# Optimization experiments

Hardware: AMD Instinct MI355X
Metric: run time of the kernel (lower is better)

The kernel has to match this reference:

```python
import jax, jax.numpy as jnp
import numpy as np

B, T, L, INPUT_DIM = 16, 128, 100, 100
EMB = 100
FEAT = INPUT_DIM + 3 * EMB          # 400
HID, OUT = 128, 50
RNN_IN = 2 * INPUT_DIM + 3 * L      # 500
VOCAB = 10000 + 2


def setup_inputs() -> dict:
    key = jax.random.key(0)
    ks = jax.random.split(key, 12)
    first = jax.random.normal(ks[0], (B, T, INPUT_DIM), jnp.float32)
    idx = jax.random.randint(ks[1], (B, T, 3 * L), 0, VOCAB).astype(jnp.float32)
    x = jnp.concatenate([first, idx], axis=2)  # [B,T,400]
    s = 0.05
    return {
        "x": x,
        "embed_nodes": jax.random.normal(ks[2], (VOCAB, EMB), jnp.float32) * s,
        "embed_paths": jax.random.normal(ks[3], (VOCAB, EMB), jnp.float32) * s,
        "W_t": jax.random.normal(ks[4], (FEAT, FEAT), jnp.float32) / np.sqrt(FEAT),
        "b_t": jnp.zeros((FEAT,), jnp.float32),
        "W_a": jax.random.normal(ks[5], (FEAT, 1), jnp.float32) / np.sqrt(FEAT),
        "b_a": jnp.zeros((1,), jnp.float32),
        "W_ih": jax.random.normal(ks[6], (4 * HID, RNN_IN), jnp.float32) / np.sqrt(RNN_IN),
        "W_hh": jax.random.normal(ks[7], (4 * HID, HID), jnp.float32) / np.sqrt(HID),
        "b_ih": jnp.zeros((4 * HID,), jnp.float32),
        "b_hh": jnp.zeros((4 * HID,), jnp.float32),
        "W_fc": jax.random.normal(ks[8], (HID, OUT), jnp.float32) / np.sqrt(HID),
        "b_fc": jnp.zeros((OUT,), jnp.float32),
    }


def _lstm(xs, W_ih, W_hh, b_ih, b_hh):
    # xs: [B,T,D] -> out [B,T,H]; PyTorch gate order i,f,g,o
    def step(carry, xt):
        h, c = carry
        g = xt @ W_ih.T + h @ W_hh.T + (b_ih + b_hh)  # [B,4H]
        i, f, gg, o = jnp.split(g, 4, axis=-1)
        c = jax.nn.sigmoid(f) * c + jax.nn.sigmoid(i) * jnp.tanh(gg)
        h = jax.nn.sigmoid(o) * jnp.tanh(c)
        return (h, c), h
    h0 = jnp.zeros((xs.shape[0], HID), xs.dtype)
    (_, _), hs = jax.lax.scan(step, (h0, h0), jnp.swapaxes(xs, 0, 1))
    return jnp.swapaxes(hs, 0, 1)


def reference(x, embed_nodes, embed_paths, W_t, b_t, W_a, b_a,
              W_ih, W_hh, b_ih, b_hh, W_fc, b_fc):
    first = x[:, :, :INPUT_DIM]                                   # [B,T,100]
    c2v = x[:, :, INPUT_DIM:INPUT_DIM + 3 * L].reshape(B, T, L, 3).astype(jnp.int32)
    s_emb = embed_nodes[c2v[..., 0]]                              # [B,T,L,100]
    e_emb = embed_nodes[c2v[..., 2]]
    p_emb = embed_paths[c2v[..., 1]]
    att_part = jnp.broadcast_to(first[:, :, None, :], (B, T, L, INPUT_DIM))
    full = jnp.concatenate([s_emb, e_emb, p_emb, att_part], axis=3)  # [B,T,L,400]
    # dropout skipped (deterministic reference == evaluating=True path)
    transformed = jnp.tanh(full @ W_t + b_t)
    ctx = transformed @ W_a + b_a                                 # [B,T,L,1]
    # faithful to nn.Softmax(dim=1): softmax over the sequence axis T
    attn = jax.nn.softmax(ctx, axis=1)
    code_vectors = jnp.sum(full * attn, axis=2)                   # [B,T,400]
    rnn_input = jnp.concatenate([first, code_vectors], axis=2)    # [B,T,500]
    out = _lstm(rnn_input, W_ih, W_hh, b_ih, b_hh)                # [B,T,128]
    return jax.nn.sigmoid(out @ W_fc + b_fc)                      # [B,T,50]
```

## Files before the change

kernel.cpp:

```cpp
#include <hip/hip_runtime.h>
#include <hip/hip_bf16.h>
#include <stdint.h>

#define B_     16
#define T_     128
#define L_     100
#define IN_    100
#define EMB_   100
#define FEAT_  400
#define HID_   128
#define OUT_   50
#define RNNIN_ 500
#define VOCAB_ 10002
#define BT_    2048
#define TBLK   157

#define S_T    (0.16f / 127.0f)
#define INVS_T (127.0f / 0.16f)

typedef __attribute__((ext_vector_type(8))) short short8;
typedef __attribute__((ext_vector_type(4))) float f32x4;

__device__ __forceinline__ float fast_tanh(float x) {
    x = fminf(15.f, fmaxf(-15.f, x));
    float e = __expf(2.f * x);
    return (e - 1.f) * __builtin_amdgcn_rcpf(e + 1.f);
}
__device__ __forceinline__ float sigm(float x) {
    x = fminf(30.f, fmaxf(-30.f, x));
    float e = __expf(-x);
    return __builtin_amdgcn_rcpf(1.f + e);
}
__device__ __forceinline__ signed char q8(float v, float invs) {
    float t = fminf(127.f, fmaxf(-127.f, v * invs));
    return (signed char)__float2int_rn(t);
}
__device__ __forceinline__ int sb(unsigned int u, int k) {
    return (int)(signed char)(u >> (8 * k));
}

__global__ __launch_bounds__(256) void casts_k(
    const float* __restrict__ Wt, const float* __restrict__ Wih,
    const float* __restrict__ Whh,
    __hip_bfloat16* __restrict__ WtT, __hip_bfloat16* __restrict__ Wih_bf,
    __hip_bfloat16* __restrict__ Whh_bf)
{
    int t0 = blockIdx.x * 256 + threadIdx.x;
    const int stride = 256 * 256;
    for (int i = t0; i < 4 * 400 * 128; i += stride) {
        int w = i / (400 * 128), rem = i - w * 400 * 128;
        int n = rem >> 7, k = rem & 127;
        WtT[i] = __float2bfloat16((k < 100) ? Wt[(size_t)(w * 100 + k) * 400 + n] : 0.f);
    }
    for (int i = t0; i < 512 * 512; i += stride) {
        int g = i >> 9, k = i & 511;
        Wih_bf[i] = __float2bfloat16((k < 500) ? Wih[(size_t)g * 500 + k] : 0.f);
    }
    for (int i = t0; i < 512 * 128; i += stride) Whh_bf[i] = __float2bfloat16(Whh[i]);
}

__device__ __forceinline__ void load_a100_f32(const float* __restrict__ arow,
                                              int kg, short8 af[4])
{
#pragma unroll
    for (int s = 0; s < 3; s++) {
        const float* p = arow + s * 32 + kg * 8;
#pragma unroll
        for (int j = 0; j < 8; j++)
            af[s][j] = (short)__bfloat16_as_ushort(__float2bfloat16(p[j]));
    }
    short8 z = {};
    af[3] = z;
    if (kg == 0) {
#pragma unroll
        for (int j = 0; j < 4; j++)
            af[3][j] = (short)__bfloat16_as_ushort(__float2bfloat16(arow[96 + j]));
    }
}

__global__ __launch_bounds__(256) void mm_k(
    const float* __restrict__ EN, const float* __restrict__ EP,
    const float* __restrict__ x, const __hip_bfloat16* __restrict__ WtT,
    const float* __restrict__ btb,
    signed char* __restrict__ Es, signed char* __restrict__ Ee,
    signed char* __restrict__ Ep, float* __restrict__ q)
{
    int blk = blockIdx.x, tid = threadIdx.x;
    int wave = tid >> 6, lane = tid & 63;
    int cl = lane & 15, kg = lane >> 4;

    if (blk < 3 * TBLK) {
        int which = blk / TBLK, mb = blk - which * TBLK;
        const float* A = (which == 2) ? EP : EN;
        signed char* outp = (which == 0) ? Es : ((which == 1) ? Ee : Ep);
        int r0 = mb * 64 + wave * 16;
        int ra = r0 + cl; if (ra > VOCAB_ - 1) ra = VOCAB_ - 1;
        short8 af[4];
        load_a100_f32(A + (size_t)ra * 100, kg, af);
        const __hip_bfloat16* Bp = WtT + (size_t)which * 400 * 128;
        for (int n0 = 0; n0 < 25; n0++) {
            const __hip_bfloat16* brow = Bp + (size_t)(n0 * 16 + cl) * 128 + kg * 8;
            f32x4 acc = (f32x4){0.f, 0.f, 0.f, 0.f};
            acc = __builtin_amdgcn_mfma_f32_16x16x32_bf16(af[0], *(const short8*)(brow), acc, 0, 0, 0);
            acc = __builtin_amdgcn_mfma_f32_16x16x32_bf16(af[1], *(const short8*)(brow + 32), acc, 0, 0, 0);
            acc = __builtin_amdgcn_mfma_f32_16x16x32_bf16(af[2], *(const short8*)(brow + 64), acc, 0, 0, 0);
            acc = __builtin_amdgcn_mfma_f32_16x16x32_bf16(af[3], *(const short8*)(brow + 96), acc, 0, 0, 0);
            int colj = n0 * 16 + cl;
#pragma unroll
            for (int r = 0; r < 4; r++) {
                int gr = r0 + kg * 4 + r;
                if (gr < VOCAB_)
                    outp[(size_t)gr * 400 + colj] = q8(acc[r], INVS_T);
            }
        }
    } else {
        int mb = blk - 3 * TBLK;
        int r0 = mb * 64 + wave * 16;
        short8 af[4];
        load_a100_f32(x + (size_t)(r0 + cl) * 400, kg, af);
        const __hip_bfloat16* Bp = WtT + (size_t)3 * 400 * 128;
        for (int n0 = 0; n0 < 25; n0++) {
            const __hip_bfloat16* brow = Bp + (size_t)(n0 * 16 + cl) * 128 + kg * 8;
            f32x4 acc = (f32x4){0.f, 0.f, 0.f, 0.f};
            acc = __builtin_amdgcn_mfma_f32_16x16x32_bf16(af[0], *(const short8*)(brow), acc, 0, 0, 0);
            acc = __builtin_amdgcn_mfma_f32_16x16x32_bf16(af[1], *(const short8*)(brow + 32), acc, 0, 0, 0);
            acc = __builtin_amdgcn_mfma_f32_16x16x32_bf16(af[2], *(const short8*)(brow + 64), acc, 0, 0, 0);
            acc = __builtin_amdgcn_mfma_f32_16x16x32_bf16(af[3], *(const short8*)(brow + 96), acc, 0, 0, 0);
            int colj = n0 * 16 + cl;
            float bb = btb[colj];
#pragma unroll
            for (int r = 0; r < 4; r++) {
                int gr = r0 + kg * 4 + r;
                q[(size_t)gr * 400 + colj] = acc[r] + bb;
            }
        }
    }
}

__global__ __launch_bounds__(256) void stage_a(
    const float* __restrict__ x,
    const signed char* __restrict__ Es8, const signed char* __restrict__ Ee8,
    const signed char* __restrict__ Ep8,
    const float* __restrict__ q, const float* __restrict__ Wa,
    float* __restrict__ ctx)
{
    __shared__ int idx_s[300];
    int bt = blockIdx.x, tid = threadIdx.x;
    const float* xr = x + (size_t)bt * 400 + 100;
    for (int i = tid; i < 300; i += 256) idx_s[i] = (int)xr[i];
    int lane = tid & 63, wave = tid >> 6;
    bool act = lane < 50;
    int j0 = lane * 8;
    float qv[8], wv[8];
    if (act) {
        float4 qa = *(const float4*)(q + (size_t)bt * 400 + j0);
        float4 qb = *(const float4*)(q + (size_t)bt * 400 + j0 + 4);
        float4 wa = *(const float4*)(Wa + j0);
        float4 wb = *(const float4*)(Wa + j0 + 4);
        qv[0]=qa.x; qv[1]=qa.y; qv[2]=qa.z; qv[3]=qa.w;
        qv[4]=qb.x; qv[5]=qb.y; qv[6]=qb.z; qv[7]=qb.w;
        wv[0]=wa.x; wv[1]=wa.y; wv[2]=wa.z; wv[3]=wa.w;
        wv[4]=wb.x; wv[5]=wb.y; wv[6]=wb.z; wv[7]=wb.w;
    } else {
#pragma unroll
        for (int jj = 0; jj < 8; jj++) { qv[jj] = 0.f; wv[jj] = 0.f; }
    }
    __syncthreads();
    for (int l = wave; l < 100; l += 4) {
        int i0 = idx_s[3 * l], i1 = idx_s[3 * l + 1], i2 = idx_s[3 * l + 2];
        float sum = 0.f;
        if (act) {
            uint2 a  = ((const uint2*)(Es8 + (size_t)i0 * 400))[lane];
            uint2 b  = ((const uint2*)(Ee8 + (size_t)i2 * 400))[lane];
            uint2 cc = ((const uint2*)(Ep8 + (size_t)i1 * 400))[lane];
            int zi[8];
#pragma unroll
            for (int k = 0; k < 4; k++) {
                zi[k]     = sb(a.x, k) + sb(b.x, k) + sb(cc.x, k);
                zi[4 + k] = sb(a.y, k) + sb(b.y, k) + sb(cc.y, k);
            }
#pragma unroll
            for (int jj = 0; jj < 8; jj++) {
                float z = fmaf((float)zi[jj], S_T, qv[jj]);
                sum = fmaf(fast_tanh(z), wv[jj], sum);
            }
        }
#pragma unroll
        for (int off = 32; off; off >>= 1) sum += __shfl_xor(sum, off);
        if (lane == 0) ctx[(size_t)bt * 100 + l] = sum;
    }
}

__global__ __launch_bounds__(256) void softmax_w(
    const float* __restrict__ ctx, float* __restrict__ attn)
{
    int wid = blockIdx.x * 4 + (threadIdx.x >> 6);
    int lane = threadIdx.x & 63;
    int b = wid / 100, l = wid - b * 100;
    size_t base = (size_t)b * 128 * 100 + l;
    float v0 = ctx[base + (size_t)lane * 100];
    float v1 = ctx[base + (size_t)(lane + 64) * 100];
    float m = fmaxf(v0, v1);
#pragma unroll
    for (int off = 32; off; off >>= 1) m = fmaxf(m, __shfl_xor(m, off));
    float e0 = __expf(v0 - m), e1 = __expf(v1 - m);
    float s = e0 + e1;
#pragma unroll
    for (int off = 32; off; off >>= 1) s += __shfl_xor(s, off);
    float rs = 1.f / s;
    attn[base + (size_t)lane * 100] = e0 * rs;
    attn[base + (size_t)(lane + 64) * 100] = e1 * rs;
}

__global__ __launch_bounds__(128) void stage_c(
    const float* __restrict__ x, const float* __restrict__ attn,
    const float* __restrict__ EN, const float* __restrict__ EP,
    __hip_bfloat16* __restrict__ rnn_bf)
{
    __shared__ float at[100];
    __shared__ int idx[300];
    int bt = blockIdx.x, tid = threadIdx.x;
    if (tid < 100) at[tid] = attn[(size_t)bt * 100 + tid];
    const float* xr = x + (size_t)bt * 400 + 100;
    for (int i = tid; i < 300; i += 128) idx[i] = (int)xr[i];
    __syncthreads();
    int d = tid;
    __hip_bfloat16* o = rnn_bf + (size_t)bt * 512;
    if (d < 100) {
        float as = 0.f, ae = 0.f, ap = 0.f, sa = 0.f;
#pragma unroll 4
        for (int l = 0; l < 100; l++) {
            float a = at[l]; sa += a;
            as = fmaf(a, EN[(size_t)idx[3 * l] * 100 + d], as);
            ae = fmaf(a, EN[(size_t)idx[3 * l + 2] * 100 + d], ae);
            ap = fmaf(a, EP[(size_t)idx[3 * l + 1] * 100 + d], ap);
        }
        float fi = x[(size_t)bt * 400 + d];
        o[d]       = __float2bfloat16(fi);
        o[100 + d] = __float2bfloat16(as);
        o[200 + d] = __float2bfloat16(ae);
        o[300 + d] = __float2bfloat16(ap);
        o[400 + d] = __float2bfloat16(fi * sa);
    } else if (d < 112) {
        o[400 + d] = __float2bfloat16(0.f);
    }
}

__global__ __launch_bounds__(256) void gemm_x(
    const __hip_bfloat16* __restrict__ rnn_bf, const __hip_bfloat16* __restrict__ Wih_bf,
    const float* __restrict__ bih, const float* __restrict__ bhh,
    float* __restrict__ X)
{
    int blk = blockIdx.x, tid = threadIdx.x;
    int wave = tid >> 6, lane = tid & 63;
    int cl = lane & 15, kg = lane >> 4;
    int r0 = blk * 64 + wave * 16;

    short8 af[16];
    const __hip_bfloat16* arow = rnn_bf + (size_t)(r0 + cl) * 512 + kg * 8;
#pragma unroll
    for (int ks = 0; ks < 16; ks++) af[ks] = *(const short8*)(arow + ks * 32);

    for (int n0 = 0; n0 < 32; n0 += 2) {
        const __hip_bfloat16* b0 = Wih_bf + (size_t)(n0 * 16 + cl) * 512 + kg * 8;
        const __hip_bfloat16* b1 = b0 + 16 * 512;
        f32x4 acA = (f32x4){0.f, 0.f, 0.f, 0.f};
        f32x4 acB = (f32x4){0.f, 0.f, 0.f, 0.f};
#pragma unroll
        for (int ks = 0; ks < 16; ks++) {
            acA = __builtin_amdgcn_mfma_f32_16x16x32_bf16(af[ks], *(const short8*)(b0 + ks * 32), acA, 0, 0, 0);
            acB = __builtin_amdgcn_mfma_f32_16x16x32_bf16(af[ks], *(const short8*)(b1 + ks * 32), acB, 0, 0, 0);
        }
        int c0 = n0 * 16 + cl, c1 = c0 + 16;
        float bi0 = bih[c0] + bhh[c0];
        float bi1 = bih[c1] + bhh[c1];
#pragma unroll
        for (int r = 0; r < 4; r++) {
            int m = r0 + kg * 4 + r;
            X[(size_t)m * 512 + c0] = acA[r] + bi0;
            X[(size_t)m * 512 + c1] = acB[r] + bi1;
        }
    }
}

__global__ __launch_bounds__(512, 1) void lstm_k(
    const float* __restrict__ X, const __hip_bfloat16* __restrict__ Whh_bf,
    float* __restrict__ hs)
{
    int b = blockIdx.x, tid = threadIdx.x;
    int wave = tid >> 6, lane = tid & 63;
    int col = lane & 15, kg = lane >> 4;

    short8 bf[4][4];
#pragma unroll
    for (int n = 0; n < 4; n++) {
        int g = n * 128 + wave * 16 + col;
#pragma unroll
        for (int kk = 0; kk < 4; kk++)
            bf[n][kk] = *(const short8*)(Whh_bf + (size_t)g * 128 + kk * 32 + kg * 8);
    }

    __shared__ __hip_bfloat16 hbuf[2][128];
    __shared__ float Xs[16][512];
    __shared__ float hsb_s[16][128];
    float c = 0.f;
    if (tid < 128) hbuf[0][tid] = __float2bfloat16(0.f);
    const float* xb = X + (size_t)b * 128 * 512;
    float* hb = hs + (size_t)b * 128 * 128;
    int j = wave * 16 + col;
    int p = 0;

    __syncthreads();

    for (int tc = 0; tc < 8; tc++) {
        {
            const float* src = xb + (size_t)tc * 16 * 512 + tid;
#pragma unroll
            for (int k = 0; k < 16; k++) Xs[k][tid] = src[k * 512];
        }
        __syncthreads();

#pragma unroll 1
        for (int ts = 0; ts < 16; ts++) {
            short8 af[4];
            short8 zz = {};
#pragma unroll
            for (int kk = 0; kk < 4; kk++) {
                af[kk] = zz;
                if (col == 0) af[kk] = *(const short8*)(&hbuf[p][0] + kk * 32 + kg * 8);
            }
            f32x4 acc[4];
#pragma unroll
            for (int n = 0; n < 4; n++) acc[n] = (f32x4){0.f, 0.f, 0.f, 0.f};
#pragma unroll
            for (int kk = 0; kk < 4; kk++)
#pragma unroll
                for (int n = 0; n < 4; n++)
                    acc[n] = __builtin_amdgcn_mfma_f32_16x16x32_bf16(af[kk], bf[n][kk], acc[n], 0, 0, 0);

            if (lane < 16) {
                float pi = acc[0][0] + Xs[ts][j];
                float pf = acc[1][0] + Xs[ts][128 + j];
                float pg = acc[2][0] + Xs[ts][256 + j];
                float po = acc[3][0] + Xs[ts][384 + j];
                c = sigm(pf) * c + sigm(pi) * fast_tanh(pg);
                float hn = sigm(po) * fast_tanh(c);
                hbuf[p ^ 1][j] = __float2bfloat16(hn);
                hsb_s[ts][j] = hn;
            }
            __syncthreads();
            p ^= 1;
        }

        {
            float* dst = hb + (size_t)tc * 16 * 128;
#pragma unroll
            for (int k = 0; k < 4; k++) {
                int i = k * 512 + tid;
                dst[i] = hsb_s[i >> 7][i & 127];
            }
        }
    }
}

__global__ __launch_bounds__(64) void fc_k(
    const float* __restrict__ hs, const float* __restrict__ Wfc,
    const float* __restrict__ bfc, float* __restrict__ out)
{
    int r0 = blockIdx.x * 4, o = threadIdx.x;
    if (o >= 50) return;
    float acc[4] = {0.f, 0.f, 0.f, 0.f};
    for (int j = 0; j < 128; j++) {
        float wv = Wfc[j * 50 + o];
#pragma unroll
        for (int r = 0; r < 4; r++)
            acc[r] = fmaf(hs[(size_t)(r0 + r) * 128 + j], wv, acc[r]);
    }
    float bb = bfc[o];
#pragma unroll
    for (int r = 0; r < 4; r++) out[(size_t)(r0 + r) * 50 + o] = sigm(acc[r] + bb);
}

extern "C" void kernel_launch(void* const* d_in, const int* in_sizes, int n_in,
                              void* d_out, int out_size, void* d_ws, size_t ws_size,
                              hipStream_t stream) {
    const float* x   = (const float*)d_in[0];
    const float* EN  = (const float*)d_in[1];
    const float* EP  = (const float*)d_in[2];
    const float* Wt  = (const float*)d_in[3];
    const float* bt  = (const float*)d_in[4];
    const float* Wa  = (const float*)d_in[5];
    const float* Wih = (const float*)d_in[7];
    const float* Whh = (const float*)d_in[8];
    const float* bih = (const float*)d_in[9];
    const float* bhh = (const float*)d_in[10];
    const float* Wfc = (const float*)d_in[11];
    const float* bfc = (const float*)d_in[12];
    float* out = (float*)d_out;

    char* ws = (char*)d_ws;
    size_t off = 0;
    auto alloc = [&](size_t bytes) -> char* {
        char* p = ws + off;
        off = (off + bytes + 255) & ~(size_t)255;
        return p;
    };
    signed char* Es  = (signed char*)alloc((size_t)VOCAB_ * 400);
    signed char* Ee  = (signed char*)alloc((size_t)VOCAB_ * 400);
    signed char* Epb = (signed char*)alloc((size_t)VOCAB_ * 400);
    __hip_bfloat16* WtT    = (__hip_bfloat16*)alloc((size_t)4 * 400 * 128 * 2);
    __hip_bfloat16* Wih_bf = (__hip_bfloat16*)alloc((size_t)512 * 512 * 2);
    __hip_bfloat16* Whh_bf = (__hip_bfloat16*)alloc((size_t)512 * 128 * 2);
    __hip_bfloat16* rnn_bf = (__hip_bfloat16*)alloc((size_t)BT_ * 512 * 2);
    float* q    = (float*)alloc((size_t)BT_ * 400 * 4);
    float* ctx  = (float*)alloc((size_t)BT_ * 100 * 4);
    float* attn = (float*)alloc((size_t)BT_ * 100 * 4);
    float* X    = (float*)alloc((size_t)BT_ * 512 * 4);
    float* hsb  = (float*)alloc((size_t)BT_ * 128 * 4);

    casts_k<<<256, 256, 0, stream>>>(Wt, Wih, Whh, WtT, Wih_bf, Whh_bf);
    mm_k<<<3 * TBLK + 32, 256, 0, stream>>>(EN, EP, x, WtT, bt,
                                            Es, Ee, Epb, q);
    stage_a<<<BT_, 256, 0, stream>>>(x, Es, Ee, Epb, q, Wa, ctx);
    softmax_w<<<400, 256, 0, stream>>>(ctx, attn);
    stage_c<<<BT_, 128, 0, stream>>>(x, attn, EN, EP, rnn_bf);
    gemm_x<<<32, 256, 0, stream>>>(rnn_bf, Wih_bf, bih, bhh, X);
    lstm_k<<<B_, 512, 0, stream>>>(X, Whh_bf, hsb);
    fc_k<<<BT_ / 4, 64, 0, stream>>>(hsb, Wfc, bfc, out);
}
```

Before: 275.0 us.

## Fold weight casts into mm_k and fuse FC epilogue into LSTM kernel

Removes the separate casts_k launch. mm_k now reads W_t directly as fp32 with strided column loads and converts to bf16 in registers, and extra blocks appended to its grid convert Wih/Whh. The fc_k kernel is removed; each LSTM block stages Wfc in shared memory after the recurrence and computes the sigmoid output for its own batch row. This saves two launches and the WtT round trip, at the cost of uncoalesced strided W_t reads repeated per block and an FC tail running on only 16 blocks.

```diff
diff --git a/kernel.cpp b/kernel.cpp
--- a/kernel.cpp
+++ b/kernel.cpp
@@ -14,6 +14,7 @@
 #define VOCAB_ 10002
 #define BT_    2048
 #define TBLK   157
+#define MMGRID (3 * TBLK + 32 + 64)
 
 #define S_T    (0.16f / 127.0f)
 #define INVS_T (127.0f / 0.16f)
@@ -39,26 +40,6 @@
     return (int)(signed char)(u >> (8 * k));
 }
 
-__global__ __launch_bounds__(256) void casts_k(
-    const float* __restrict__ Wt, const float* __restrict__ Wih,
-    const float* __restrict__ Whh,
-    __hip_bfloat16* __restrict__ WtT, __hip_bfloat16* __restrict__ Wih_bf,
-    __hip_bfloat16* __restrict__ Whh_bf)
-{
-    int t0 = blockIdx.x * 256 + threadIdx.x;
-    const int stride = 256 * 256;
-    for (int i = t0; i < 4 * 400 * 128; i += stride) {
-        int w = i / (400 * 128), rem = i - w * 400 * 128;
-        int n = rem >> 7, k = rem & 127;
-        WtT[i] = __float2bfloat16((k < 100) ? Wt[(size_t)(w * 100 + k) * 400 + n] : 0.f);
-    }
-    for (int i = t0; i < 512 * 512; i += stride) {
-        int g = i >> 9, k = i & 511;
-        Wih_bf[i] = __float2bfloat16((k < 500) ? Wih[(size_t)g * 500 + k] : 0.f);
-    }
-    for (int i = t0; i < 512 * 128; i += stride) Whh_bf[i] = __float2bfloat16(Whh[i]);
-}
-
 __device__ __forceinline__ void load_a100_f32(const float* __restrict__ arow,
                                               int kg, short8 af[4])
 {
@@ -78,12 +59,33 @@
     }
 }
 
+__device__ __forceinline__ void load_b100_f32(const float* __restrict__ colbase,
+                                              int kg, short8 bfr[4])
+{
+#pragma unroll
+    for (int s = 0; s < 3; s++) {
+        const float* p = colbase + (size_t)(s * 32 + kg * 8) * 400;
+#pragma unroll
+        for (int j = 0; j < 8; j++)
+            bfr[s][j] = (short)__bfloat16_as_ushort(__float2bfloat16(p[(size_t)j * 400]));
+    }
+    short8 z = {};
+    bfr[3] = z;
+    if (kg == 0) {
+#pragma unroll
+        for (int j = 0; j < 4; j++)
+            bfr[3][j] = (short)__bfloat16_as_ushort(__float2bfloat16(colbase[(size_t)(96 + j) * 400]));
+    }
+}
+
 __global__ __launch_bounds__(256) void mm_k(
     const float* __restrict__ EN, const float* __restrict__ EP,
-    const float* __restrict__ x, const __hip_bfloat16* __restrict__ WtT,
+    const float* __restrict__ x, const float* __restrict__ Wt,
     const float* __restrict__ btb,
+    const float* __restrict__ Wih, const float* __restrict__ Whh,
     signed char* __restrict__ Es, signed char* __restrict__ Ee,
-    signed char* __restrict__ Ep, float* __restrict__ q)
+    signed char* __restrict__ Ep, float* __restrict__ q,
+    __hip_bfloat16* __restrict__ Wih_bf, __hip_bfloat16* __restrict__ Whh_bf)
 {
     int blk = blockIdx.x, tid = threadIdx.x;
     int wave = tid >> 6, lane = tid & 63;
@@ -97,15 +99,16 @@
         int ra = r0 + cl; if (ra > VOCAB_ - 1) ra = VOCAB_ - 1;
         short8 af[4];
         load_a100_f32(A + (size_t)ra * 100, kg, af);
-        const __hip_bfloat16* Bp = WtT + (size_t)which * 400 * 128;
+        const float* Wslice = Wt + (size_t)(which * 100) * 400;
         for (int n0 = 0; n0 < 25; n0++) {
-            const __hip_bfloat16* brow = Bp + (size_t)(n0 * 16 + cl) * 128 + kg * 8;
+            int colj = n0 * 16 + cl;
+            short8 bfr[4];
+            load_b100_f32(Wslice + colj, kg, bfr);
             f32x4 acc = (f32x4){0.f, 0.f, 0.f, 0.f};
-            acc = __builtin_amdgcn_mfma_f32_16x16x32_bf16(af[0], *(const short8*)(brow), acc, 0, 0, 0);
-            acc = __builtin_amdgcn_mfma_f32_16x16x32_bf16(af[1], *(const short8*)(brow + 32), acc, 0, 0, 0);
-            acc = __builtin_amdgcn_mfma_f32_16x16x32_bf16(af[2], *(const short8*)(brow + 64), acc, 0, 0, 0);
-            acc = __builtin_amdgcn_mfma_f32_16x16x32_bf16(af[3], *(const short8*)(brow + 96), acc, 0, 0, 0);
-            int colj = n0 * 16 + cl;
+            acc = __builtin_amdgcn_mfma_f32_16x16x32_bf16(af[0], bfr[0], acc, 0, 0, 0);
+            acc = __builtin_amdgcn_mfma_f32_16x16x32_bf16(af[1], bfr[1], acc, 0, 0, 0);
+            acc = __builtin_amdgcn_mfma_f32_16x16x32_bf16(af[2], bfr[2], acc, 0, 0, 0);
+            acc = __builtin_amdgcn_mfma_f32_16x16x32_bf16(af[3], bfr[3], acc, 0, 0, 0);
 #pragma unroll
             for (int r = 0; r < 4; r++) {
                 int gr = r0 + kg * 4 + r;
@@ -113,20 +116,21 @@
                     outp[(size_t)gr * 400 + colj] = q8(acc[r], INVS_T);
             }
         }
-    } else {
+    } else if (blk < 3 * TBLK + 32) {
         int mb = blk - 3 * TBLK;
         int r0 = mb * 64 + wave * 16;
         short8 af[4];
         load_a100_f32(x + (size_t)(r0 + cl) * 400, kg, af);
-        const __hip_bfloat16* Bp = WtT + (size_t)3 * 400 * 128;
+        const float* Wslice = Wt + (size_t)300 * 400;
         for (int n0 = 0; n0 < 25; n0++) {
-            const __hip_bfloat16* brow = Bp + (size_t)(n0 * 16 + cl) * 128 + kg * 8;
+            int colj = n0 * 16 + cl;
+            short8 bfr[4];
+            load_b100_f32(Wslice + colj, kg, bfr);
             f32x4 acc = (f32x4){0.f, 0.f, 0.f, 0.f};
-            acc = __builtin_amdgcn_mfma_f32_16x16x32_bf16(af[0], *(const short8*)(brow), acc, 0, 0, 0);
-            acc = __builtin_amdgcn_mfma_f32_16x16x32_bf16(af[1], *(const short8*)(brow + 32), acc, 0, 0, 0);
-            acc = __builtin_amdgcn_mfma_f32_16x16x32_bf16(af[2], *(const short8*)(brow + 64), acc, 0, 0, 0);
-            acc = __builtin_amdgcn_mfma_f32_16x16x32_bf16(af[3], *(const short8*)(brow + 96), acc, 0, 0, 0);
-            int colj = n0 * 16 + cl;
+            acc = __builtin_amdgcn_mfma_f32_16x16x32_bf16(af[0], bfr[0], acc, 0, 0, 0);
+            acc = __builtin_amdgcn_mfma_f32_16x16x32_bf16(af[1], bfr[1], acc, 0, 0, 0);
+            acc = __builtin_amdgcn_mfma_f32_16x16x32_bf16(af[2], bfr[2], acc, 0, 0, 0);
+            acc = __builtin_amdgcn_mfma_f32_16x16x32_bf16(af[3], bfr[3], acc, 0, 0, 0);
             float bb = btb[colj];
 #pragma unroll
             for (int r = 0; r < 4; r++) {
@@ -134,6 +138,16 @@
                 q[(size_t)gr * 400 + colj] = acc[r] + bb;
             }
         }
+    } else {
+        int cb = blk - (3 * TBLK + 32);
+        int t0 = cb * 256 + tid;
+        const int stride = 64 * 256;
+        for (int i = t0; i < 512 * 512; i += stride) {
+            int g = i >> 9, k = i & 511;
+            Wih_bf[i] = __float2bfloat16((k < 500) ? Wih[(size_t)g * 500 + k] : 0.f);
+        }
+        for (int i = t0; i < 512 * 128; i += stride)
+            Whh_bf[i] = __float2bfloat16(Whh[i]);
     }
 }
 
@@ -285,7 +299,8 @@
 
 __global__ __launch_bounds__(512, 1) void lstm_k(
     const float* __restrict__ X, const __hip_bfloat16* __restrict__ Whh_bf,
-    float* __restrict__ hs)
+    const float* __restrict__ Wfc, const float* __restrict__ bfc,
+    float* __restrict__ hs, float* __restrict__ out)
 {
     int b = blockIdx.x, tid = threadIdx.x;
     int wave = tid >> 6, lane = tid & 63;
@@ -361,24 +376,25 @@
             }
         }
     }
-}
-
-__global__ __launch_bounds__(64) void fc_k(
-    const float* __restrict__ hs, const float* __restrict__ Wfc,
-    const float* __restrict__ bfc, float* __restrict__ out)
-{
-    int r0 = blockIdx.x * 4, o = threadIdx.x;
-    if (o >= 50) return;
-    float acc[4] = {0.f, 0.f, 0.f, 0.f};
-    for (int j = 0; j < 128; j++) {
-        float wv = Wfc[j * 50 + o];
-#pragma unroll
-        for (int r = 0; r < 4; r++)
-            acc[r] = fmaf(hs[(size_t)(r0 + r) * 128 + j], wv, acc[r]);
-    }
-    float bb = bfc[o];
-#pragma unroll
-    for (int r = 0; r < 4; r++) out[(size_t)(r0 + r) * 50 + o] = sigm(acc[r] + bb);
+
+    __syncthreads();
+    float* wfc_s = (float*)&Xs[0][0];
+    for (int i = tid; i < 6400; i += 512) wfc_s[i] = Wfc[i];
+    __syncthreads();
+    for (int i = tid; i < 128 * 50; i += 512) {
+        int t = i / 50, o = i - t * 50;
+        float acc = bfc[o];
+        const float4* h4 = (const float4*)(hb + (size_t)t * 128);
+#pragma unroll 8
+        for (int q4 = 0; q4 < 32; q4++) {
+            float4 hv = h4[q4];
+            acc = fmaf(hv.x, wfc_s[(q4 * 4 + 0) * 50 + o], acc);
+            acc = fmaf(hv.y, wfc_s[(q4 * 4 + 1) * 50 + o], acc);
+            acc = fmaf(hv.z, wfc_s[(q4 * 4 + 2) * 50 + o], acc);
+            acc = fmaf(hv.w, wfc_s[(q4 * 4 + 3) * 50 + o], acc);
+        }
+        out[((size_t)b * 128 + t) * 50 + o] = sigm(acc);
+    }
 }
 
 extern "C" void kernel_launch(void* const* d_in, const int* in_sizes, int n_in,
@@ -408,7 +424,6 @@
     signed char* Es  = (signed char*)alloc((size_t)VOCAB_ * 400);
     signed char* Ee  = (signed char*)alloc((size_t)VOCAB_ * 400);
     signed char* Epb = (signed char*)alloc((size_t)VOCAB_ * 400);
-    __hip_bfloat16* WtT    = (__hip_bfloat16*)alloc((size_t)4 * 400 * 128 * 2);
     __hip_bfloat16* Wih_bf = (__hip_bfloat16*)alloc((size_t)512 * 512 * 2);
     __hip_bfloat16* Whh_bf = (__hip_bfloat16*)alloc((size_t)512 * 128 * 2);
     __hip_bfloat16* rnn_bf = (__hip_bfloat16*)alloc((size_t)BT_ * 512 * 2);
@@ -418,13 +433,11 @@
     float* X    = (float*)alloc((size_t)BT_ * 512 * 4);
     float* hsb  = (float*)alloc((size_t)BT_ * 128 * 4);
 
-    casts_k<<<256, 256, 0, stream>>>(Wt, Wih, Whh, WtT, Wih_bf, Whh_bf);
-    mm_k<<<3 * TBLK + 32, 256, 0, stream>>>(EN, EP, x, WtT, bt,
-                                            Es, Ee, Epb, q);
+    mm_k<<<MMGRID, 256, 0, stream>>>(EN, EP, x, Wt, bt, Wih, Whh,
+                                     Es, Ee, Epb, q, Wih_bf, Whh_bf);
     stage_a<<<BT_, 256, 0, stream>>>(x, Es, Ee, Epb, q, Wa, ctx);
     softmax_w<<<400, 256, 0, stream>>>(ctx, attn);
     stage_c<<<BT_, 128, 0, stream>>>(x, attn, EN, EP, rnn_bf);
     gemm_x<<<32, 256, 0, stream>>>(rnn_bf, Wih_bf, bih, bhh, X);
-    lstm_k<<<B_, 512, 0, stream>>>(X, Whh_bf, hsb);
-    fc_k<<<BT_ / 4, 64, 0, stream>>>(hsb, Wfc, bfc, out);
-}
+    lstm_k<<<B_, 512, 0, stream>>>(X, Whh_bf, Wfc, bfc, hsb, out);
+}
```

Result: slower. 294.9 us (+7.2%).
